# Kernel optimization log

Hardware: AMD Instinct MI355X
Metric: run time of the kernel (lower is better)

Reference implementation:

```python
import jax, jax.numpy as jnp
import numpy as np
from jax import lax

B, T, D = 8, 4096, 1024


def setup_inputs() -> dict:
    key = jax.random.key(0)
    ks = jax.random.split(key, 8)
    s = 1.0 / np.sqrt(D)  # keep GEMM outputs O(1)
    return {
        "x": jax.random.normal(ks[0], (B, T, D), dtype=jnp.float32),
        "state_p": jnp.zeros((B, D), dtype=jnp.float32),
        "decay": 0.8 + 0.19 * jax.random.uniform(ks[1], (D,), dtype=jnp.float32),  # ~0.9, stable
        "mass": jnp.ones((D,), dtype=jnp.float32),
        "Wq": s * jax.random.normal(ks[2], (D, D), dtype=jnp.float32),
        "bq": jnp.zeros((D,), dtype=jnp.float32),
        "Wk": s * jax.random.normal(ks[3], (D, D), dtype=jnp.float32),
        "bk": jnp.zeros((D,), dtype=jnp.float32),
        "Wv": s * jax.random.normal(ks[4], (D, D), dtype=jnp.float32),
        "bv": jnp.zeros((D,), dtype=jnp.float32),
    }


def reference(x, state_p, decay, mass, Wq, bq, Wk, bk, Wv, bv):
    # Batch all per-timestep projections into single GEMMs over (B*T) tokens.
    k_logit = jnp.einsum("btd,ed->bte", x, Wk) + bk        # [B,T,D]
    v = jnp.einsum("btd,ed->bte", x, Wv) + bv              # [B,T,D]
    u = jax.nn.sigmoid(k_logit) * v                          # gated input, [B,T,D]

    # Diagonal linear recurrence p_t = decay * p_{t-1} + u_t via scan over time.
    def step(p, u_t):
        p = p * decay + u_t
        return p, p

    final_p, ps = lax.scan(step, state_p, jnp.swapaxes(u, 0, 1))  # ps: [T,B,D]
    p = jnp.swapaxes(ps, 0, 1)                                     # [B,T,D]

    velocities = (jnp.einsum("btd,ed->bte", p, Wq) + bq) / mass    # [B,T,D]
    return velocities, final_p
```

## Files before the change

### kernel.cpp

```cpp
#include <hip/hip_runtime.h>
#include <stdint.h>
#include <stddef.h>

#define D_DIM 1024
#define T_LEN 4096
#define B_SZ 8
#define M_ROWS 32768
#define KTOT 1024
#define CHUNK 64
#define NCHUNK 64

typedef unsigned short u16;
typedef unsigned short u16x8 __attribute__((ext_vector_type(8)));
typedef __bf16 bf16x8 __attribute__((ext_vector_type(8)));
typedef float f32x4 __attribute__((ext_vector_type(4)));

__device__ __forceinline__ u16 f2bf(float f) {
    union { float f; unsigned u; } v; v.f = f;
    unsigned r = v.u + 0x7fffu + ((v.u >> 16) & 1u);
    return (u16)(r >> 16);
}
__device__ __forceinline__ float bf2f(u16 h) {
    union { unsigned u; float f; } v; v.u = ((unsigned)h) << 16;
    return v.f;
}

__global__ void convert_kernel(const float* __restrict__ src, u16* __restrict__ dst, int n4) {
    int i = blockIdx.x * blockDim.x + threadIdx.x;
    int stride = gridDim.x * blockDim.x;
    for (int j = i; j < n4; j += stride) {
        float4 v = ((const float4*)src)[j];
        ushort4 o;
        o.x = f2bf(v.x); o.y = f2bf(v.y); o.z = f2bf(v.z); o.w = f2bf(v.w);
        ((ushort4*)dst)[j] = o;
    }
}

__global__ void convert_w_kernel(const float* __restrict__ Wk, const float* __restrict__ Wv,
                                 const float* __restrict__ Wq,
                                 u16* __restrict__ wcat, u16* __restrict__ wqb) {
    int total = 3072 * 256;
    int stride = gridDim.x * blockDim.x;
    for (int idx = blockIdx.x * blockDim.x + threadIdx.x; idx < total; idx += stride) {
        int r = idx >> 8, c4 = idx & 255;
        const float* src; u16* dst;
        if (r < 2048) {
            int g = r >> 5, j = r & 31;
            src = (j < 16 ? Wk : Wv) + (size_t)(g * 16 + (j & 15)) * D_DIM;
            dst = wcat + (size_t)r * D_DIM;
        } else {
            src = Wq + (size_t)(r - 2048) * D_DIM;
            dst = wqb + (size_t)(r - 2048) * D_DIM;
        }
        float4 v = ((const float4*)src)[c4];
        ushort4 o;
        o.x = f2bf(v.x); o.y = f2bf(v.y); o.z = f2bf(v.z); o.w = f2bf(v.w);
        ((ushort4*)dst)[c4] = o;
    }
}

__device__ __forceinline__ void gload16(const u16* g, u16* l) {
    __builtin_amdgcn_global_load_lds(
        (const __attribute__((address_space(1))) void*)g,
        (__attribute__((address_space(3))) void*)l,
        16, 0, 0);
}

template<bool CAT>
__global__ __launch_bounds__(512, 2) void gemm5_kernel(
    const u16* __restrict__ A,
    const u16* __restrict__ Bg,
    const float* __restrict__ bias0,
    const float* __restrict__ bias1,
    u16* __restrict__ Uout,
    float* __restrict__ Fout)
{
    constexpr int NT = KTOT / 64;
    __shared__ u16 smem[2 * 32768];

    const int tid  = threadIdx.x;
    const int w    = tid >> 6;
    const int lane = tid & 63;

    const int cpx = gridDim.x >> 3;
    const int swz = (blockIdx.x & 7) * cpx + (blockIdx.x >> 3);
    const int nCol = CAT ? 8 : 4;
    const int M0 = (swz / nCol) * 256;
    const int N0 = (swz % nCol) * 256;

    const int srow = lane >> 2;
    const int sg   = (lane & 3) ^ ((srow >> 1) & 3);

    const u16* pA0 = A  + (size_t)(M0 + w * 32 +      srow) * KTOT + sg * 8;
    const u16* pA1 = A  + (size_t)(M0 + w * 32 + 16 + srow) * KTOT + sg * 8;
    const u16* pB0 = Bg + (size_t)(N0 + w * 32 +      srow) * KTOT + sg * 8;
    const u16* pB1 = Bg + (size_t)(N0 + w * 32 + 16 + srow) * KTOT + sg * 8;

    auto stA = [&](u16* nxt, int h) {
        gload16(pA0, nxt + h * 8192 + w * 1024);       pA0 += 32;
        gload16(pA1, nxt + h * 8192 + w * 1024 + 512); pA1 += 32;
    };
    auto stB = [&](u16* nxt, int h) {
        gload16(pB0, nxt + 16384 + h * 8192 + w * 1024);       pB0 += 32;
        gload16(pB1, nxt + 16384 + h * 8192 + w * 1024 + 512); pB1 += 32;
    };

    const int wrow = (w >> 2) * 128;
    const int wcol = (w & 3) * 64;
    const int fr = lane & 15;
    const int fq = lane >> 4;

    int offA[8], offB[4];
#pragma unroll
    for (int m = 0; m < 8; ++m) {
        int row = wrow + m * 16 + fr;
        offA[m] = row * 32 + ((fq ^ ((row >> 1) & 3)) << 3);
    }
#pragma unroll
    for (int n = 0; n < 4; ++n) {
        int row = wcol + n * 16 + fr;
        offB[n] = 16384 + row * 32 + ((fq ^ ((row >> 1) & 3)) << 3);
    }

    f32x4 acc[8][4] = {};

    stA(smem, 0); stB(smem, 0); stA(smem, 1); stB(smem, 1);
    asm volatile("s_waitcnt vmcnt(4)" ::: "memory");
    __builtin_amdgcn_s_barrier();

#pragma unroll 1
    for (int t = 0; t < NT; ++t) {
        const u16* cur = smem + (t & 1) * 32768;
        u16* nxt = smem + ((t + 1) & 1) * 32768;
        const bool pf = (t + 1 < NT);

        bf16x8 aA[4], aB[4], bA[4], aC[4], aD[4], bC[4];

#pragma unroll
        for (int n = 0; n < 4; ++n) bA[n] = *(const bf16x8*)(cur + offB[n]);
#pragma unroll
        for (int m = 0; m < 4; ++m) aA[m] = *(const bf16x8*)(cur + offA[m]);
        if (pf) stA(nxt, 0);
        __builtin_amdgcn_s_barrier();
        asm volatile("s_waitcnt lgkmcnt(0)" ::: "memory");
        __builtin_amdgcn_sched_barrier(0);
        __builtin_amdgcn_s_setprio(1);
#pragma unroll
        for (int m = 0; m < 4; ++m)
#pragma unroll
            for (int n = 0; n < 4; ++n)
                acc[m][n] = __builtin_amdgcn_mfma_f32_16x16x32_bf16(aA[m], bA[n], acc[m][n], 0, 0, 0);
        __builtin_amdgcn_s_setprio(0);
        __builtin_amdgcn_sched_barrier(0);
        __builtin_amdgcn_s_barrier();

#pragma unroll
        for (int m = 0; m < 4; ++m) aB[m] = *(const bf16x8*)(cur + offA[4 + m]);
        if (pf) stB(nxt, 0);
        __builtin_amdgcn_s_barrier();
        asm volatile("s_waitcnt lgkmcnt(0)" ::: "memory");
        __builtin_amdgcn_sched_barrier(0);
        __builtin_amdgcn_s_setprio(1);
#pragma unroll
        for (int m = 0; m < 4; ++m)
#pragma unroll
            for (int n = 0; n < 4; ++n)
                acc[4 + m][n] = __builtin_amdgcn_mfma_f32_16x16x32_bf16(aB[m], bA[n], acc[4 + m][n], 0, 0, 0);
        __builtin_amdgcn_s_setprio(0);
        __builtin_amdgcn_sched_barrier(0);
        if (pf) { asm volatile("s_waitcnt vmcnt(4)" ::: "memory"); }
        else    { asm volatile("s_waitcnt vmcnt(0)" ::: "memory"); }
        __builtin_amdgcn_s_barrier();

#pragma unroll
        for (int n = 0; n < 4; ++n) bC[n] = *(const bf16x8*)(cur + 8192 + offB[n]);
#pragma unroll
        for (int m = 0; m < 4; ++m) aC[m] = *(const bf16x8*)(cur + 8192 + offA[m]);
        if (pf) stA(nxt, 1);
        __builtin_amdgcn_s_barrier();
        asm volatile("s_waitcnt lgkmcnt(0)" ::: "memory");
        __builtin_amdgcn_sched_barrier(0);
        __builtin_amdgcn_s_setprio(1);
#pragma unroll
        for (int m = 0; m < 4; ++m)
#pragma unroll
            for (int n = 0; n < 4; ++n)
                acc[m][n] = __builtin_amdgcn_mfma_f32_16x16x32_bf16(aC[m], bC[n], acc[m][n], 0, 0, 0);
        __builtin_amdgcn_s_setprio(0);
        __builtin_amdgcn_sched_barrier(0);
        __builtin_amdgcn_s_barrier();

#pragma unroll
        for (int m = 0; m < 4; ++m) aD[m] = *(const bf16x8*)(cur + 8192 + offA[4 + m]);
        if (pf) stB(nxt, 1);
        __builtin_amdgcn_s_barrier();
        asm volatile("s_waitcnt lgkmcnt(0)" ::: "memory");
        __builtin_amdgcn_sched_barrier(0);
        __builtin_amdgcn_s_setprio(1);
#pragma unroll
        for (int m = 0; m < 4; ++m)
#pragma unroll
            for (int n = 0; n < 4; ++n)
                acc[4 + m][n] = __builtin_amdgcn_mfma_f32_16x16x32_bf16(aD[m], bC[n], acc[4 + m][n], 0, 0, 0);
        __builtin_amdgcn_s_setprio(0);
        __builtin_amdgcn_sched_barrier(0);
        if (pf) { asm volatile("s_waitcnt vmcnt(4)" ::: "memory"); }
        __builtin_amdgcn_s_barrier();
    }

    if (CAT) {
        const int ucol0 = N0 / 2 + (w & 3) * 32;
#pragma unroll
        for (int p = 0; p < 2; ++p) {
            int col = ucol0 + p * 16 + fr;
            float b0 = bias0[col];
            float b1 = bias1[col];
#pragma unroll
            for (int m = 0; m < 8; ++m) {
                int row0 = M0 + wrow + m * 16 + fq * 4;
#pragma unroll
                for (int j = 0; j < 4; ++j) {
                    float kl = acc[m][2 * p][j] + b0;
                    float vv = acc[m][2 * p + 1][j] + b1;
                    float sig = 1.0f / (1.0f + __expf(-kl));
                    Uout[(size_t)(row0 + j) * D_DIM + col] = f2bf(sig * vv);
                }
            }
        }
    } else {
#pragma unroll
        for (int n = 0; n < 4; ++n) {
            int col = N0 + wcol + n * 16 + fr;
            float b0 = bias0[col];
            float b1 = bias1[col];
#pragma unroll
            for (int m = 0; m < 8; ++m) {
                int row0 = M0 + wrow + m * 16 + fq * 4;
#pragma unroll
                for (int j = 0; j < 4; ++j)
                    Fout[(size_t)(row0 + j) * D_DIM + col] = (acc[m][n][j] + b0) / b1;
            }
        }
    }
}

__global__ void chunk_carry_kernel(const u16* __restrict__ u, const float* __restrict__ decay,
                                   float* __restrict__ localc) {
    int id = blockIdx.x * blockDim.x + threadIdx.x;
    int d8 = id & 127;
    int c  = (id >> 7) & (NCHUNK - 1);
    int b  = id >> 13;
    float4 dlo = ((const float4*)decay)[d8 * 2];
    float4 dhi = ((const float4*)decay)[d8 * 2 + 1];
    float dec[8] = {dlo.x, dlo.y, dlo.z, dlo.w, dhi.x, dhi.y, dhi.z, dhi.w};
    float carry[8] = {};
    const u16* up = u + ((size_t)b * T_LEN + (size_t)c * CHUNK) * D_DIM + d8 * 8;
    for (int s = 0; s < CHUNK; ++s) {
        u16x8 v = *(const u16x8*)(up + (size_t)s * D_DIM);
#pragma unroll
        for (int j = 0; j < 8; ++j)
            carry[j] = fmaf(carry[j], dec[j], bf2f(v[j]));
    }
    float* lc = localc + ((size_t)(b * NCHUNK + c)) * D_DIM + d8 * 8;
#pragma unroll
    for (int j = 0; j < 8; ++j) lc[j] = carry[j];
}

__global__ void carry_scan_kernel(const float* __restrict__ localc, const float* __restrict__ state_p,
                                  const float* __restrict__ decay, float* __restrict__ prefix,
                                  float* __restrict__ final_p) {
    int id = blockIdx.x * blockDim.x + threadIdx.x;
    int d = id & (D_DIM - 1);
    int b = id >> 10;
    float dec = decay[d];
    float dl = dec;
#pragma unroll
    for (int i = 0; i < 6; ++i) dl *= dl;
    float P = state_p[id];
    for (int c = 0; c < NCHUNK; ++c) {
        int idx = (b * NCHUNK + c) * D_DIM + d;
        prefix[idx] = P;
        P = fmaf(P, dl, localc[idx]);
    }
    final_p[id] = P;
}

__global__ void reconstruct_kernel(u16* __restrict__ u, const float* __restrict__ decay,
                                   const float* __restrict__ prefix) {
    int id = blockIdx.x * blockDim.x + threadIdx.x;
    int d8 = id & 127;
    int c  = (id >> 7) & (NCHUNK - 1);
    int b  = id >> 13;
    float4 dlo = ((const float4*)decay)[d8 * 2];
    float4 dhi = ((const float4*)decay)[d8 * 2 + 1];
    float dec[8] = {dlo.x, dlo.y, dlo.z, dlo.w, dhi.x, dhi.y, dhi.z, dhi.w};
    const float* pf = prefix + ((size_t)(b * NCHUNK + c)) * D_DIM + d8 * 8;
    float p[8];
#pragma unroll
    for (int j = 0; j < 8; ++j) p[j] = pf[j];
    u16* up = u + ((size_t)b * T_LEN + (size_t)c * CHUNK) * D_DIM + d8 * 8;
    for (int s = 0; s < CHUNK; ++s) {
        u16x8 v = *(const u16x8*)(up + (size_t)s * D_DIM);
        u16x8 o;
#pragma unroll
        for (int j = 0; j < 8; ++j) {
            p[j] = fmaf(p[j], dec[j], bf2f(v[j]));
            o[j] = f2bf(p[j]);
        }
        *(u16x8*)(up + (size_t)s * D_DIM) = o;
    }
}

extern "C" void kernel_launch(void* const* d_in, const int* in_sizes, int n_in,
                              void* d_out, int out_size, void* d_ws, size_t ws_size,
                              hipStream_t stream) {
    const float* x       = (const float*)d_in[0];
    const float* state_p = (const float*)d_in[1];
    const float* decay   = (const float*)d_in[2];
    const float* mass    = (const float*)d_in[3];
    const float* Wq      = (const float*)d_in[4];
    const float* bq      = (const float*)d_in[5];
    const float* Wk      = (const float*)d_in[6];
    const float* bk      = (const float*)d_in[7];
    const float* Wv      = (const float*)d_in[8];
    const float* bv      = (const float*)d_in[9];

    float* out     = (float*)d_out;
    float* final_p = out + (size_t)M_ROWS * D_DIM;

    u16* xb = (u16*)d_out;

    u16* wcat = (u16*)d_ws;
    u16* wqb  = wcat + 2048 * 1024;
    u16* ub   = wqb + 1024 * 1024;
    float* localc = (float*)(ub + (size_t)M_ROWS * D_DIM);
    float* prefix = localc + B_SZ * NCHUNK * D_DIM;

    convert_kernel<<<4096, 256, 0, stream>>>(x, xb, (M_ROWS * D_DIM) / 4);
    convert_w_kernel<<<1536, 256, 0, stream>>>(Wk, Wv, Wq, wcat, wqb);

    gemm5_kernel<true><<<dim3(1024), dim3(512), 0, stream>>>(
        xb, wcat, bk, bv, ub, nullptr);

    chunk_carry_kernel<<<256, 256, 0, stream>>>(ub, decay, localc);
    carry_scan_kernel<<<32, 256, 0, stream>>>(localc, state_p, decay, prefix, final_p);
    reconstruct_kernel<<<256, 256, 0, stream>>>(ub, decay, prefix);

    gemm5_kernel<false><<<dim3(512), dim3(512), 0, stream>>>(
        ub, wqb, bq, mass, nullptr, out);
}
```

Measured before the change: 309.0 us.

## Software-pipeline LDS fragment loads one phase ahead in GEMM main loop

Restructures the GEMM inner loop so each LDS fragment load for the next MFMA phase is issued before the current phase's MFMAs, with the next tile's first fragments preloaded at the end of each iteration. Per-phase s_barrier/lgkmcnt waits drop from eight to two per iteration, and the vmcnt thresholds are adjusted. The goal is to hide LDS read latency behind MFMA work and cut barrier stalls. The cost is higher register pressure from keeping more fragment buffers live, and a risk of LDS read/write hazards now that fewer barriers guard the double buffer.

```diff
diff --git a/kernel.cpp b/kernel.cpp
--- a/kernel.cpp
+++ b/kernel.cpp
@@ -66,8 +66,10 @@
         16, 0, 0);
 }
 
+#define SBAR() __builtin_amdgcn_sched_barrier(0)
+
 template<bool CAT>
-__global__ __launch_bounds__(512, 2) void gemm5_kernel(
+__global__ __launch_bounds__(512, 2) void gemm6_kernel(
     const u16* __restrict__ A,
     const u16* __restrict__ Bg,
     const float* __restrict__ bias0,
@@ -123,10 +125,15 @@
     }
 
     f32x4 acc[8][4] = {};
+    bf16x8 aA[4], aB[4], aC[4], aD[4], bA[4], bC[4];
 
     stA(smem, 0); stB(smem, 0); stA(smem, 1); stB(smem, 1);
     asm volatile("s_waitcnt vmcnt(4)" ::: "memory");
     __builtin_amdgcn_s_barrier();
+#pragma unroll
+    for (int m = 0; m < 4; ++m) aA[m] = *(const bf16x8*)(smem + offA[m]);
+#pragma unroll
+    for (int n = 0; n < 4; ++n) bA[n] = *(const bf16x8*)(smem + offB[n]);
 
 #pragma unroll 1
     for (int t = 0; t < NT; ++t) {
@@ -134,16 +141,10 @@
         u16* nxt = smem + ((t + 1) & 1) * 32768;
         const bool pf = (t + 1 < NT);
 
-        bf16x8 aA[4], aB[4], bA[4], aC[4], aD[4], bC[4];
-
-#pragma unroll
-        for (int n = 0; n < 4; ++n) bA[n] = *(const bf16x8*)(cur + offB[n]);
-#pragma unroll
-        for (int m = 0; m < 4; ++m) aA[m] = *(const bf16x8*)(cur + offA[m]);
+#pragma unroll
+        for (int m = 0; m < 4; ++m) aB[m] = *(const bf16x8*)(cur + offA[4 + m]);
         if (pf) stA(nxt, 0);
-        __builtin_amdgcn_s_barrier();
-        asm volatile("s_waitcnt lgkmcnt(0)" ::: "memory");
-        __builtin_amdgcn_sched_barrier(0);
+        SBAR();
         __builtin_amdgcn_s_setprio(1);
 #pragma unroll
         for (int m = 0; m < 4; ++m)
@@ -151,15 +152,17 @@
             for (int n = 0; n < 4; ++n)
                 acc[m][n] = __builtin_amdgcn_mfma_f32_16x16x32_bf16(aA[m], bA[n], acc[m][n], 0, 0, 0);
         __builtin_amdgcn_s_setprio(0);
-        __builtin_amdgcn_sched_barrier(0);
+        SBAR();
+
+        if (pf) { asm volatile("s_waitcnt vmcnt(2)" ::: "memory"); }
+        else    { asm volatile("s_waitcnt vmcnt(0)" ::: "memory"); }
         __builtin_amdgcn_s_barrier();
-
-#pragma unroll
-        for (int m = 0; m < 4; ++m) aB[m] = *(const bf16x8*)(cur + offA[4 + m]);
+#pragma unroll
+        for (int m = 0; m < 4; ++m) aC[m] = *(const bf16x8*)(cur + 8192 + offA[m]);
+#pragma unroll
+        for (int n = 0; n < 4; ++n) bC[n] = *(const bf16x8*)(cur + 8192 + offB[n]);
         if (pf) stB(nxt, 0);
-        __builtin_amdgcn_s_barrier();
-        asm volatile("s_waitcnt lgkmcnt(0)" ::: "memory");
-        __builtin_amdgcn_sched_barrier(0);
+        SBAR();
         __builtin_amdgcn_s_setprio(1);
 #pragma unroll
         for (int m = 0; m < 4; ++m)
@@ -167,19 +170,12 @@
             for (int n = 0; n < 4; ++n)
                 acc[4 + m][n] = __builtin_amdgcn_mfma_f32_16x16x32_bf16(aB[m], bA[n], acc[4 + m][n], 0, 0, 0);
         __builtin_amdgcn_s_setprio(0);
-        __builtin_amdgcn_sched_barrier(0);
-        if (pf) { asm volatile("s_waitcnt vmcnt(4)" ::: "memory"); }
-        else    { asm volatile("s_waitcnt vmcnt(0)" ::: "memory"); }
-        __builtin_amdgcn_s_barrier();
-
-#pragma unroll
-        for (int n = 0; n < 4; ++n) bC[n] = *(const bf16x8*)(cur + 8192 + offB[n]);
-#pragma unroll
-        for (int m = 0; m < 4; ++m) aC[m] = *(const bf16x8*)(cur + 8192 + offA[m]);
+        SBAR();
+
+#pragma unroll
+        for (int m = 0; m < 4; ++m) aD[m] = *(const bf16x8*)(cur + 8192 + offA[4 + m]);
         if (pf) stA(nxt, 1);
-        __builtin_amdgcn_s_barrier();
-        asm volatile("s_waitcnt lgkmcnt(0)" ::: "memory");
-        __builtin_amdgcn_sched_barrier(0);
+        SBAR();
         __builtin_amdgcn_s_setprio(1);
 #pragma unroll
         for (int m = 0; m < 4; ++m)
@@ -187,15 +183,18 @@
             for (int n = 0; n < 4; ++n)
                 acc[m][n] = __builtin_amdgcn_mfma_f32_16x16x32_bf16(aC[m], bC[n], acc[m][n], 0, 0, 0);
         __builtin_amdgcn_s_setprio(0);
-        __builtin_amdgcn_sched_barrier(0);
+        SBAR();
+
+        if (pf) { asm volatile("s_waitcnt vmcnt(2)" ::: "memory"); }
         __builtin_amdgcn_s_barrier();
-
-#pragma unroll
-        for (int m = 0; m < 4; ++m) aD[m] = *(const bf16x8*)(cur + 8192 + offA[4 + m]);
-        if (pf) stB(nxt, 1);
-        __builtin_amdgcn_s_barrier();
-        asm volatile("s_waitcnt lgkmcnt(0)" ::: "memory");
-        __builtin_amdgcn_sched_barrier(0);
+        if (pf) {
+#pragma unroll
+            for (int m = 0; m < 4; ++m) aA[m] = *(const bf16x8*)(nxt + offA[m]);
+#pragma unroll
+            for (int n = 0; n < 4; ++n) bA[n] = *(const bf16x8*)(nxt + offB[n]);
+            stB(nxt, 1);
+        }
+        SBAR();
         __builtin_amdgcn_s_setprio(1);
 #pragma unroll
         for (int m = 0; m < 4; ++m)
@@ -203,9 +202,7 @@
             for (int n = 0; n < 4; ++n)
                 acc[4 + m][n] = __builtin_amdgcn_mfma_f32_16x16x32_bf16(aD[m], bC[n], acc[4 + m][n], 0, 0, 0);
         __builtin_amdgcn_s_setprio(0);
-        __builtin_amdgcn_sched_barrier(0);
-        if (pf) { asm volatile("s_waitcnt vmcnt(4)" ::: "memory"); }
-        __builtin_amdgcn_s_barrier();
+        SBAR();
     }
 
     if (CAT) {
@@ -339,13 +336,13 @@
     convert_kernel<<<4096, 256, 0, stream>>>(x, xb, (M_ROWS * D_DIM) / 4);
     convert_w_kernel<<<1536, 256, 0, stream>>>(Wk, Wv, Wq, wcat, wqb);
 
-    gemm5_kernel<true><<<dim3(1024), dim3(512), 0, stream>>>(
+    gemm6_kernel<true><<<dim3(1024), dim3(512), 0, stream>>>(
         xb, wcat, bk, bv, ub, nullptr);
 
     chunk_carry_kernel<<<256, 256, 0, stream>>>(ub, decay, localc);
     carry_scan_kernel<<<32, 256, 0, stream>>>(localc, state_p, decay, prefix, final_p);
     reconstruct_kernel<<<256, 256, 0, stream>>>(ub, decay, prefix);
 
-    gemm5_kernel<false><<<dim3(512), dim3(512), 0, stream>>>(
+    gemm6_kernel<false><<<dim3(512), dim3(512), 0, stream>>>(
         ub, wqb, bq, mass, nullptr, out);
 }
```

Result: faster. 301.8 us (-2.3%).
